# Performance work log

Hardware: AMD Instinct MI355X
Metric: run time of the kernel (lower is better)

The kernel has to match this reference:

```python
import jax, jax.numpy as jnp
import numpy as np

BATCH = 64
N_FEAT = 50000
UNITS = 1024
NNZ = 2_000_000


def setup_inputs() -> dict:
    key = jax.random.key(0)
    k1, k2, k3, k4 = jax.random.split(key, 4)
    x = jax.random.normal(k1, (BATCH, N_FEAT), dtype=jnp.float32)
    # one trainable weight per nonzero of the sparse kernel
    w = jax.random.normal(k2, (NNZ,), dtype=jnp.float32) * 0.02
    row_idx = jax.random.randint(k3, (NNZ,), 0, N_FEAT, dtype=jnp.int32)
    col_idx = jax.random.randint(k4, (NNZ,), 0, UNITS, dtype=jnp.int32)
    return {"x": x, "w": w, "row_idx": row_idx, "col_idx": col_idx}


def reference(x, w, row_idx, col_idx):
    # out[b, u] = sum_{k : col_idx[k]==u} x[b, row_idx[k]] * w[k]
    # == tf.sparse.sparse_dense_matmul(x, SparseTensor(indices, w, [N_FEAT, UNITS]))
    vals = x[:, row_idx] * w  # [batch, nnz] gather + elementwise scale
    out = jnp.zeros((x.shape[0], UNITS), dtype=x.dtype).at[:, col_idx].add(vals)
    return out
```

## Files before the change

### kernel.cpp

```cpp
#include <hip/hip_runtime.h>
#include <hip/hip_bf16.h>

#define BATCH 64
#define UNITS 1024
#define CHUNK 8192
#define JB 32
#define NSPLIT 4

typedef unsigned int u32;
typedef unsigned short u16;

__global__ __launch_bounds__(256)
void zero4_kernel(uint4* __restrict__ p, int n4) {
    int i = blockIdx.x * 256 + threadIdx.x;
    const int stride = gridDim.x * 256;
    const uint4 z = make_uint4(0u, 0u, 0u, 0u);
    for (; i < n4; i += stride) p[i] = z;
}

__global__ __launch_bounds__(256)
void prep_kernel(const float* __restrict__ x, u16* __restrict__ xT,
                 const int* __restrict__ col, u32* __restrict__ hist2,
                 int nfeat, int nT, int nnz) {
    __shared__ float tile[64][65];
    __shared__ u32 lh[UNITS];
    const int bid = blockIdx.x;
    const int tid = threadIdx.x;
    if (bid < nT) {
        const int c0 = bid * 64;
        const int tx = tid & 63, ty = tid >> 6;
        for (int b = ty; b < 64; b += 4) {
            int c = c0 + tx;
            if (c < nfeat) tile[b][tx] = x[(size_t)b * nfeat + c];
        }
        __syncthreads();
        for (int i = ty; i < 64; i += 4) {
            int c = c0 + i;
            if (c < nfeat) {
                __hip_bfloat16 h = __float2bfloat16(tile[tx][i]);
                xT[(size_t)c * 64 + tx] = *(u16*)&h;
            }
        }
    } else {
        const int g = bid - nT;
        for (int i = tid; i < UNITS; i += 256) lh[i] = 0u;
        __syncthreads();
        const int g0 = g * CHUNK;
        const int n = min(CHUNK, nnz - g0);
        for (int i = tid; i < n; i += 256)
            atomicAdd(&lh[col[g0 + i]], 1u);
        __syncthreads();
        for (int c = tid; c < UNITS; c += 256)
            hist2[(size_t)g * UNITS + c] = lh[c];
    }
}

__global__ __launch_bounds__(1024)
void scanA_kernel(const u32* __restrict__ hist2, u32* __restrict__ partial,
                  int nchunk) {
    const int j = blockIdx.x, c = threadIdx.x;
    const int gs = j * JB, ge = min(gs + JB, nchunk);
    u32 s = 0;
#pragma unroll 8
    for (int g = gs; g < ge; ++g) s += hist2[(size_t)g * UNITS + c];
    partial[(size_t)j * UNITS + c] = s;
}

__global__ __launch_bounds__(1024)
void scanB_kernel(const u32* __restrict__ partial, u32* __restrict__ jb,
                  u32* __restrict__ col_start, int nblk) {
    const int c = threadIdx.x;
    u32 tot = 0;
    for (int j = 0; j < nblk; ++j) tot += partial[(size_t)j * UNITS + c];
    __shared__ u32 a[UNITS];
    a[c] = tot;
    __syncthreads();
    for (int off = 1; off < UNITS; off <<= 1) {
        u32 add = (c >= off) ? a[c - off] : 0u;
        u32 v = a[c];
        __syncthreads();
        a[c] = v + add;
        __syncthreads();
    }
    u32 run = a[c] - tot;
    col_start[c] = run;
    if (c == UNITS - 1) col_start[UNITS] = a[UNITS - 1];
    for (int j = 0; j < nblk; ++j) {
        jb[(size_t)j * UNITS + c] = run;
        run += partial[(size_t)j * UNITS + c];
    }
}

__global__ __launch_bounds__(512)
void reorder_kernel(const int* __restrict__ row, const int* __restrict__ col,
                    const float* __restrict__ w, const u32* __restrict__ hist2,
                    const u32* __restrict__ jb, u32* __restrict__ sorted, int nnz) {
    __shared__ u32 cur[UNITS];
    const int tid = threadIdx.x;
    const int g = blockIdx.x;
    const int j = g / JB, gs = j * JB;
    for (int c = tid; c < UNITS; c += 512) {
        u32 v = jb[(size_t)j * UNITS + c];
#pragma unroll 4
        for (int gp = gs; gp < g; ++gp) v += hist2[(size_t)gp * UNITS + c];
        cur[c] = v;
    }
    __syncthreads();
    const int g0 = g * CHUNK;
    const int n = min(CHUNK, nnz - g0);
    if (n == CHUNK) {
        for (int j2 = 0; j2 < CHUNK / 512; j2 += 8) {
            u32 cc[8], pk[8], lo[8];
#pragma unroll
            for (int q = 0; q < 8; ++q) {
                const int k = g0 + tid + 512 * (j2 + q);
                cc[q] = (u32)col[k];
                __hip_bfloat16 h = __float2bfloat16(w[k]);
                pk[q] = ((u32)(*(const u16*)&h) << 16) | (u32)row[k];
            }
#pragma unroll
            for (int q = 0; q < 8; ++q) lo[q] = atomicAdd(&cur[cc[q]], 1u);
#pragma unroll
            for (int q = 0; q < 8; ++q) sorted[lo[q]] = pk[q];
        }
    } else {
        for (int i = tid; i < n; i += 512) {
            const int k = g0 + i;
            const u32 c = (u32)col[k];
            __hip_bfloat16 h = __float2bfloat16(w[k]);
            const u32 pk = ((u32)(*(const u16*)&h) << 16) | (u32)row[k];
            const u32 lo = atomicAdd(&cur[c], 1u);
            sorted[lo] = pk;
        }
    }
}

__global__ __launch_bounds__(256)
void gather_kernel(const u16* __restrict__ xTu, const u32* __restrict__ sorted,
                   const u32* __restrict__ col_start, float* __restrict__ out) {
    const int u = blockIdx.x >> 2;
    const int part = blockIdx.x & 3;
    const int tid = threadIdx.x;
    const int wv = tid >> 6, lane = tid & 63;
    const u32 s = col_start[u], e = col_start[u + 1];
    float acc0 = 0.f, acc1 = 0.f, acc2 = 0.f, acc3 = 0.f;
    for (u32 b0 = s + (u32)(part * 4 + wv) * 64u; b0 < e; b0 += (u32)(NSPLIT * 4) * 64u) {
        u32 pk = 0u;
        if (b0 + (u32)lane < e) pk = sorted[b0 + (u32)lane];
#pragma unroll
        for (int t = 0; t < 64; t += 4) {
            const u32 e0 = (u32)__builtin_amdgcn_readlane((int)pk, t);
            const u32 e1 = (u32)__builtin_amdgcn_readlane((int)pk, t + 1);
            const u32 e2 = (u32)__builtin_amdgcn_readlane((int)pk, t + 2);
            const u32 e3 = (u32)__builtin_amdgcn_readlane((int)pk, t + 3);
            const u16* p0 = xTu + ((e0 & 0xffffu) << 6);
            const u16* p1 = xTu + ((e1 & 0xffffu) << 6);
            const u16* p2 = xTu + ((e2 & 0xffffu) << 6);
            const u16* p3 = xTu + ((e3 & 0xffffu) << 6);
            const float x0 = __uint_as_float(((u32)p0[lane]) << 16);
            const float x1 = __uint_as_float(((u32)p1[lane]) << 16);
            const float x2 = __uint_as_float(((u32)p2[lane]) << 16);
            const float x3 = __uint_as_float(((u32)p3[lane]) << 16);
            acc0 = fmaf(x0, __uint_as_float(e0 & 0xffff0000u), acc0);
            acc1 = fmaf(x1, __uint_as_float(e1 & 0xffff0000u), acc1);
            acc2 = fmaf(x2, __uint_as_float(e2 & 0xffff0000u), acc2);
            acc3 = fmaf(x3, __uint_as_float(e3 & 0xffff0000u), acc3);
        }
    }
    float tot = (acc0 + acc1) + (acc2 + acc3);
    __shared__ float red[4][64];
    red[wv][lane] = tot;
    __syncthreads();
    if (wv == 0)
        unsafeAtomicAdd(&out[(size_t)lane * UNITS + u],
                        red[0][lane] + red[1][lane] + red[2][lane] + red[3][lane]);
}

__global__ __launch_bounds__(1024, 1)
void scatter_fallback_kernel(const u16* __restrict__ xT, const float* __restrict__ w,
                             const int* __restrict__ row_idx, const int* __restrict__ col_idx,
                             float* __restrict__ out, int nnz) {
    extern __shared__ float priv[];
    const int tid = threadIdx.x;
    for (int i = tid; i < 32 * UNITS; i += 1024) priv[i] = 0.0f;
    __syncthreads();
    const int bid = blockIdx.x, half = bid >> 7, wgIdx = bid & 127;
    const int wave = tid >> 6, lane = tid & 63, h = lane >> 5, bl = lane & 31;
    const int per = (nnz + 127) >> 7;
    const int k0 = wgIdx * per, kend = min(k0 + per, nnz);
    const u16* xTh = xT + half * 32 + bl;
    for (int k = k0 + wave * 2 + h; k < kend; k += 32) {
        const int r = row_idx[k], c = col_idx[k];
        const float xv = __uint_as_float(((u32)xTh[(size_t)r * 64]) << 16);
        atomicAdd(&priv[c * 32 + bl], xv * w[k]);
    }
    __syncthreads();
    for (int i = tid; i < 32 * UNITS; i += 1024) {
        int c = i >> 5, b = half * 32 + (i & 31);
        unsafeAtomicAdd(&out[b * UNITS + c], priv[i]);
    }
}

__global__ __launch_bounds__(256)
void fallback_kernel(const float* __restrict__ x, const float* __restrict__ w,
                     const int* __restrict__ row_idx, const int* __restrict__ col_idx,
                     float* __restrict__ out, int nnz, int nfeat) {
    const int nwaves = (gridDim.x * blockDim.x) >> 6;
    const int wid = (blockIdx.x * blockDim.x + threadIdx.x) >> 6;
    const int lane = threadIdx.x & 63;
    for (int k = wid; k < nnz; k += nwaves) {
        const int r = row_idx[k], c = col_idx[k];
        unsafeAtomicAdd(&out[lane * UNITS + c], x[(size_t)lane * nfeat + r] * w[k]);
    }
}

static inline size_t align256(size_t v) { return (v + 255) & ~(size_t)255; }

extern "C" void kernel_launch(void* const* d_in, const int* in_sizes, int n_in,
                              void* d_out, int out_size, void* d_ws, size_t ws_size,
                              hipStream_t stream) {
    const float* x       = (const float*)d_in[0];
    const float* w       = (const float*)d_in[1];
    const int*   row_idx = (const int*)d_in[2];
    const int*   col_idx = (const int*)d_in[3];
    float*       out     = (float*)d_out;
    const int    nnz     = in_sizes[1];
    const int    nfeat   = in_sizes[0] / BATCH;
    const int    nchunk  = (nnz + CHUNK - 1) / CHUNK;
    const int    nblk    = (nchunk + JB - 1) / JB;
    const int    nT      = (nfeat + 63) / 64;

    const size_t xT_bytes = (size_t)nfeat * 64 * sizeof(u16);
    size_t o = align256(xT_bytes);
    const size_t sorted_off = o;  o = align256(o + (size_t)nnz * sizeof(u32));
    const size_t hist2_off  = o;  o = align256(o + (size_t)nchunk * UNITS * sizeof(u32));
    const size_t part_off   = o;  o = align256(o + (size_t)nblk * UNITS * sizeof(u32));
    const size_t jb_off     = o;  o = align256(o + (size_t)nblk * UNITS * sizeof(u32));
    const size_t cs_off     = o;  o = align256(o + (UNITS + 1) * sizeof(u32));

    const int nOut4 = (out_size * 4 + 15) / 16;

    if (ws_size >= o && nfeat <= 65536 && nblk <= 64) {
        u16* xT        = (u16*)d_ws;
        u32* sorted    = (u32*)((char*)d_ws + sorted_off);
        u32* hist2     = (u32*)((char*)d_ws + hist2_off);
        u32* partial   = (u32*)((char*)d_ws + part_off);
        u32* jb        = (u32*)((char*)d_ws + jb_off);
        u32* col_start = (u32*)((char*)d_ws + cs_off);

        zero4_kernel<<<64, 256, 0, stream>>>((uint4*)out, nOut4);
        prep_kernel<<<nT + nchunk, 256, 0, stream>>>(x, xT, col_idx, hist2,
                                                     nfeat, nT, nnz);
        scanA_kernel<<<nblk, 1024, 0, stream>>>(hist2, partial, nchunk);
        scanB_kernel<<<1, 1024, 0, stream>>>(partial, jb, col_start, nblk);
        reorder_kernel<<<nchunk, 512, 0, stream>>>(row_idx, col_idx, w, hist2,
                                                   jb, sorted, nnz);
        gather_kernel<<<UNITS * NSPLIT, 256, 0, stream>>>(xT, sorted, col_start, out);
    } else if (ws_size >= xT_bytes) {
        u16* xT = (u16*)d_ws;
        zero4_kernel<<<64, 256, 0, stream>>>((uint4*)out, nOut4);
        prep_kernel<<<nT, 256, 0, stream>>>(x, xT, col_idx, nullptr, nfeat, nT, 0);
        scatter_fallback_kernel<<<256, 1024, 32 * UNITS * sizeof(float), stream>>>(
            xT, w, row_idx, col_idx, out, nnz);
    } else {
        zero4_kernel<<<64, 256, 0, stream>>>((uint4*)out, nOut4);
        fallback_kernel<<<2048, 256, 0, stream>>>(x, w, row_idx, col_idx, out, nnz, nfeat);
    }
}
```

Measured before the change: 146.2 us.

## Fold output zeroing into prep kernel and merge two-level scan into one

New measurement: 166.1 us. +13.7%, slower.

```diff
diff --git a/kernel.cpp b/kernel.cpp
--- a/kernel.cpp
+++ b/kernel.cpp
@@ -4,8 +4,8 @@
 #define BATCH 64
 #define UNITS 1024
 #define CHUNK 8192
-#define JB 32
 #define NSPLIT 4
+#define NZERO 16
 
 typedef unsigned int u32;
 typedef unsigned short u16;
@@ -21,13 +21,18 @@
 __global__ __launch_bounds__(256)
 void prep_kernel(const float* __restrict__ x, u16* __restrict__ xT,
                  const int* __restrict__ col, u32* __restrict__ hist2,
-                 int nfeat, int nT, int nnz) {
+                 float* __restrict__ out, int nfeat, int nZ, int nT, int nnz) {
     __shared__ float tile[64][65];
     __shared__ u32 lh[UNITS];
     const int bid = blockIdx.x;
     const int tid = threadIdx.x;
-    if (bid < nT) {
-        const int c0 = bid * 64;
+    if (bid < nZ) {
+        uint4* o4 = (uint4*)out;
+        const uint4 z = make_uint4(0u, 0u, 0u, 0u);
+        const int n4 = (BATCH * UNITS) / 4;
+        for (int i = bid * 256 + tid; i < n4; i += nZ * 256) o4[i] = z;
+    } else if (bid < nZ + nT) {
+        const int c0 = (bid - nZ) * 64;
         const int tx = tid & 63, ty = tid >> 6;
         for (int b = ty; b < 64; b += 4) {
             int c = c0 + tx;
@@ -42,7 +47,7 @@
             }
         }
     } else {
-        const int g = bid - nT;
+        const int g = bid - nZ - nT;
         for (int i = tid; i < UNITS; i += 256) lh[i] = 0u;
         __syncthreads();
         const int g0 = g * CHUNK;
@@ -56,22 +61,23 @@
 }
 
 __global__ __launch_bounds__(1024)
-void scanA_kernel(const u32* __restrict__ hist2, u32* __restrict__ partial,
-                  int nchunk) {
-    const int j = blockIdx.x, c = threadIdx.x;
-    const int gs = j * JB, ge = min(gs + JB, nchunk);
-    u32 s = 0;
-#pragma unroll 8
-    for (int g = gs; g < ge; ++g) s += hist2[(size_t)g * UNITS + c];
-    partial[(size_t)j * UNITS + c] = s;
-}
-
-__global__ __launch_bounds__(1024)
-void scanB_kernel(const u32* __restrict__ partial, u32* __restrict__ jb,
-                  u32* __restrict__ col_start, int nblk) {
+void scan_kernel(const u32* __restrict__ hist2, u32* __restrict__ base2,
+                 u32* __restrict__ col_start, int nchunk) {
     const int c = threadIdx.x;
     u32 tot = 0;
-    for (int j = 0; j < nblk; ++j) tot += partial[(size_t)j * UNITS + c];
+    int g = 0;
+    for (; g + 8 <= nchunk; g += 8) {
+        u32 h0 = hist2[(size_t)(g + 0) * UNITS + c];
+        u32 h1 = hist2[(size_t)(g + 1) * UNITS + c];
+        u32 h2 = hist2[(size_t)(g + 2) * UNITS + c];
+        u32 h3 = hist2[(size_t)(g + 3) * UNITS + c];
+        u32 h4 = hist2[(size_t)(g + 4) * UNITS + c];
+        u32 h5 = hist2[(size_t)(g + 5) * UNITS + c];
+        u32 h6 = hist2[(size_t)(g + 6) * UNITS + c];
+        u32 h7 = hist2[(size_t)(g + 7) * UNITS + c];
+        tot += ((h0 + h1) + (h2 + h3)) + ((h4 + h5) + (h6 + h7));
+    }
+    for (; g < nchunk; ++g) tot += hist2[(size_t)g * UNITS + c];
     __shared__ u32 a[UNITS];
     a[c] = tot;
     __syncthreads();
@@ -85,26 +91,32 @@
     u32 run = a[c] - tot;
     col_start[c] = run;
     if (c == UNITS - 1) col_start[UNITS] = a[UNITS - 1];
-    for (int j = 0; j < nblk; ++j) {
-        jb[(size_t)j * UNITS + c] = run;
-        run += partial[(size_t)j * UNITS + c];
+    g = 0;
+    for (; g + 4 <= nchunk; g += 4) {
+        u32 h0 = hist2[(size_t)(g + 0) * UNITS + c];
+        u32 h1 = hist2[(size_t)(g + 1) * UNITS + c];
+        u32 h2 = hist2[(size_t)(g + 2) * UNITS + c];
+        u32 h3 = hist2[(size_t)(g + 3) * UNITS + c];
+        base2[(size_t)(g + 0) * UNITS + c] = run; run += h0;
+        base2[(size_t)(g + 1) * UNITS + c] = run; run += h1;
+        base2[(size_t)(g + 2) * UNITS + c] = run; run += h2;
+        base2[(size_t)(g + 3) * UNITS + c] = run; run += h3;
+    }
+    for (; g < nchunk; ++g) {
+        base2[(size_t)g * UNITS + c] = run;
+        run += hist2[(size_t)g * UNITS + c];
     }
 }
 
 __global__ __launch_bounds__(512)
 void reorder_kernel(const int* __restrict__ row, const int* __restrict__ col,
-                    const float* __restrict__ w, const u32* __restrict__ hist2,
-                    const u32* __restrict__ jb, u32* __restrict__ sorted, int nnz) {
+                    const float* __restrict__ w, const u32* __restrict__ base2,
+                    u32* __restrict__ sorted, int nnz) {
     __shared__ u32 cur[UNITS];
     const int tid = threadIdx.x;
     const int g = blockIdx.x;
-    const int j = g / JB, gs = j * JB;
-    for (int c = tid; c < UNITS; c += 512) {
-        u32 v = jb[(size_t)j * UNITS + c];
-#pragma unroll 4
-        for (int gp = gs; gp < g; ++gp) v += hist2[(size_t)gp * UNITS + c];
-        cur[c] = v;
-    }
+    for (int c = tid; c < UNITS; c += 512)
+        cur[c] = base2[(size_t)g * UNITS + c];
     __syncthreads();
     const int g0 = g * CHUNK;
     const int n = min(CHUNK, nnz - g0);
@@ -227,39 +239,34 @@
     const int    nnz     = in_sizes[1];
     const int    nfeat   = in_sizes[0] / BATCH;
     const int    nchunk  = (nnz + CHUNK - 1) / CHUNK;
-    const int    nblk    = (nchunk + JB - 1) / JB;
     const int    nT      = (nfeat + 63) / 64;
 
     const size_t xT_bytes = (size_t)nfeat * 64 * sizeof(u16);
     size_t o = align256(xT_bytes);
     const size_t sorted_off = o;  o = align256(o + (size_t)nnz * sizeof(u32));
     const size_t hist2_off  = o;  o = align256(o + (size_t)nchunk * UNITS * sizeof(u32));
-    const size_t part_off   = o;  o = align256(o + (size_t)nblk * UNITS * sizeof(u32));
-    const size_t jb_off     = o;  o = align256(o + (size_t)nblk * UNITS * sizeof(u32));
+    const size_t base2_off  = o;  o = align256(o + (size_t)nchunk * UNITS * sizeof(u32));
     const size_t cs_off     = o;  o = align256(o + (UNITS + 1) * sizeof(u32));
 
     const int nOut4 = (out_size * 4 + 15) / 16;
 
-    if (ws_size >= o && nfeat <= 65536 && nblk <= 64) {
+    if (ws_size >= o && nfeat <= 65536 && nchunk <= 4096) {
         u16* xT        = (u16*)d_ws;
         u32* sorted    = (u32*)((char*)d_ws + sorted_off);
         u32* hist2     = (u32*)((char*)d_ws + hist2_off);
-        u32* partial   = (u32*)((char*)d_ws + part_off);
-        u32* jb        = (u32*)((char*)d_ws + jb_off);
+        u32* base2     = (u32*)((char*)d_ws + base2_off);
         u32* col_start = (u32*)((char*)d_ws + cs_off);
 
-        zero4_kernel<<<64, 256, 0, stream>>>((uint4*)out, nOut4);
-        prep_kernel<<<nT + nchunk, 256, 0, stream>>>(x, xT, col_idx, hist2,
-                                                     nfeat, nT, nnz);
-        scanA_kernel<<<nblk, 1024, 0, stream>>>(hist2, partial, nchunk);
-        scanB_kernel<<<1, 1024, 0, stream>>>(partial, jb, col_start, nblk);
-        reorder_kernel<<<nchunk, 512, 0, stream>>>(row_idx, col_idx, w, hist2,
-                                                   jb, sorted, nnz);
+        prep_kernel<<<NZERO + nT + nchunk, 256, 0, stream>>>(
+            x, xT, col_idx, hist2, out, nfeat, NZERO, nT, nnz);
+        scan_kernel<<<1, 1024, 0, stream>>>(hist2, base2, col_start, nchunk);
+        reorder_kernel<<<nchunk, 512, 0, stream>>>(row_idx, col_idx, w, base2,
+                                                   sorted, nnz);
         gather_kernel<<<UNITS * NSPLIT, 256, 0, stream>>>(xT, sorted, col_start, out);
     } else if (ws_size >= xT_bytes) {
         u16* xT = (u16*)d_ws;
-        zero4_kernel<<<64, 256, 0, stream>>>((uint4*)out, nOut4);
-        prep_kernel<<<nT, 256, 0, stream>>>(x, xT, col_idx, nullptr, nfeat, nT, 0);
+        prep_kernel<<<NZERO + nT, 256, 0, stream>>>(
+            x, xT, col_idx, nullptr, out, nfeat, NZERO, nT, 0);
         scatter_fallback_kernel<<<256, 1024, 32 * UNITS * sizeof(float), stream>>>(
             xT, w, row_idx, col_idx, out, nnz);
     } else {
```

## Split gather by batch halves, one block per column, drop atomics and zeroing

Applied to the files above, without the earlier changes.

After: 162.9 us. 1.11x slower.

```diff
diff --git a/kernel.cpp b/kernel.cpp
--- a/kernel.cpp
+++ b/kernel.cpp
@@ -5,7 +5,6 @@
 #define UNITS 1024
 #define CHUNK 8192
 #define JB 32
-#define NSPLIT 4
 
 typedef unsigned int u32;
 typedef unsigned short u16;
@@ -135,45 +134,49 @@
     }
 }
 
-__global__ __launch_bounds__(256)
-void gather_kernel(const u16* __restrict__ xTu, const u32* __restrict__ sorted,
-                   const u32* __restrict__ col_start, float* __restrict__ out) {
-    const int u = blockIdx.x >> 2;
-    const int part = blockIdx.x & 3;
-    const int tid = threadIdx.x;
-    const int wv = tid >> 6, lane = tid & 63;
+template<int HALF>
+__global__ __launch_bounds__(256)
+void gather_half_kernel(const u16* __restrict__ xTu, const u32* __restrict__ sorted,
+                        const u32* __restrict__ col_start, float* __restrict__ out) {
+    const int u = blockIdx.x;
+    const int tid = threadIdx.x;
+    const int wv = tid >> 6;
+    const int lane = tid & 63;
+    const int sub = lane >> 5;
+    const int bl = lane & 31;
     const u32 s = col_start[u], e = col_start[u + 1];
+    const u16* xh = xTu + HALF * 32 + bl;
     float acc0 = 0.f, acc1 = 0.f, acc2 = 0.f, acc3 = 0.f;
-    for (u32 b0 = s + (u32)(part * 4 + wv) * 64u; b0 < e; b0 += (u32)(NSPLIT * 4) * 64u) {
+    for (u32 b0 = s + (u32)wv * 64u; b0 < e; b0 += 256u) {
         u32 pk = 0u;
         if (b0 + (u32)lane < e) pk = sorted[b0 + (u32)lane];
 #pragma unroll
-        for (int t = 0; t < 64; t += 4) {
-            const u32 e0 = (u32)__builtin_amdgcn_readlane((int)pk, t);
-            const u32 e1 = (u32)__builtin_amdgcn_readlane((int)pk, t + 1);
-            const u32 e2 = (u32)__builtin_amdgcn_readlane((int)pk, t + 2);
-            const u32 e3 = (u32)__builtin_amdgcn_readlane((int)pk, t + 3);
-            const u16* p0 = xTu + ((e0 & 0xffffu) << 6);
-            const u16* p1 = xTu + ((e1 & 0xffffu) << 6);
-            const u16* p2 = xTu + ((e2 & 0xffffu) << 6);
-            const u16* p3 = xTu + ((e3 & 0xffffu) << 6);
-            const float x0 = __uint_as_float(((u32)p0[lane]) << 16);
-            const float x1 = __uint_as_float(((u32)p1[lane]) << 16);
-            const float x2 = __uint_as_float(((u32)p2[lane]) << 16);
-            const float x3 = __uint_as_float(((u32)p3[lane]) << 16);
-            acc0 = fmaf(x0, __uint_as_float(e0 & 0xffff0000u), acc0);
-            acc1 = fmaf(x1, __uint_as_float(e1 & 0xffff0000u), acc1);
-            acc2 = fmaf(x2, __uint_as_float(e2 & 0xffff0000u), acc2);
-            acc3 = fmaf(x3, __uint_as_float(e3 & 0xffff0000u), acc3);
+        for (int t = 0; t < 64; t += 8) {
+            u32 ee[4];
+#pragma unroll
+            for (int q = 0; q < 4; ++q) {
+                const u32 ea = (u32)__builtin_amdgcn_readlane((int)pk, t + 2 * q);
+                const u32 eb = (u32)__builtin_amdgcn_readlane((int)pk, t + 2 * q + 1);
+                ee[q] = sub ? eb : ea;
+            }
+            float xv[4];
+#pragma unroll
+            for (int q = 0; q < 4; ++q)
+                xv[q] = __uint_as_float(((u32)xh[(size_t)(ee[q] & 0xffffu) << 6]) << 16);
+            acc0 = fmaf(xv[0], __uint_as_float(ee[0] & 0xffff0000u), acc0);
+            acc1 = fmaf(xv[1], __uint_as_float(ee[1] & 0xffff0000u), acc1);
+            acc2 = fmaf(xv[2], __uint_as_float(ee[2] & 0xffff0000u), acc2);
+            acc3 = fmaf(xv[3], __uint_as_float(ee[3] & 0xffff0000u), acc3);
         }
     }
     float tot = (acc0 + acc1) + (acc2 + acc3);
-    __shared__ float red[4][64];
-    red[wv][lane] = tot;
-    __syncthreads();
-    if (wv == 0)
-        unsafeAtomicAdd(&out[(size_t)lane * UNITS + u],
-                        red[0][lane] + red[1][lane] + red[2][lane] + red[3][lane]);
+    tot += __shfl_xor(tot, 32);
+    __shared__ float red[4][32];
+    if (sub == 0) red[wv][bl] = tot;
+    __syncthreads();
+    if (tid < 32)
+        out[(size_t)(HALF * 32 + tid) * UNITS + u] =
+            red[0][tid] + red[1][tid] + red[2][tid] + red[3][tid];
 }
 
 __global__ __launch_bounds__(1024, 1)
@@ -248,14 +251,14 @@
         u32* jb        = (u32*)((char*)d_ws + jb_off);
         u32* col_start = (u32*)((char*)d_ws + cs_off);
 
-        zero4_kernel<<<64, 256, 0, stream>>>((uint4*)out, nOut4);
         prep_kernel<<<nT + nchunk, 256, 0, stream>>>(x, xT, col_idx, hist2,
                                                      nfeat, nT, nnz);
         scanA_kernel<<<nblk, 1024, 0, stream>>>(hist2, partial, nchunk);
         scanB_kernel<<<1, 1024, 0, stream>>>(partial, jb, col_start, nblk);
         reorder_kernel<<<nchunk, 512, 0, stream>>>(row_idx, col_idx, w, hist2,
                                                    jb, sorted, nnz);
-        gather_kernel<<<UNITS * NSPLIT, 256, 0, stream>>>(xT, sorted, col_start, out);
+        gather_half_kernel<0><<<UNITS, 256, 0, stream>>>(xT, sorted, col_start, out);
+        gather_half_kernel<1><<<UNITS, 256, 0, stream>>>(xT, sorted, col_start, out);
     } else if (ws_size >= xT_bytes) {
         u16* xT = (u16*)d_ws;
         zero4_kernel<<<64, 256, 0, stream>>>((uint4*)out, nOut4);
```
